# Performance work log

Hardware: AMD Instinct MI355X
Metric: run time of the kernel (lower is better)

## Reference

```python
import jax, jax.numpy as jnp
import numpy as np

N, D, V, T = 1024, 64, 32000, 2048
U_DECAY = 0.97
LN_EPS = 1e-6


def _layernorm_row(z):
    # matches torch: (z - mean) / (std_unbiased + eps), std uses ddof=1
    m = z.mean(axis=-1, keepdims=True)
    s = jnp.std(z, axis=-1, ddof=1, keepdims=True)
    return (z - m) / (s + LN_EPS)


def setup_inputs() -> dict:
    key = jax.random.key(0)
    k1, k2, k3, k4, k5 = jax.random.split(key, 5)
    E = jax.random.normal(k1, (D, N), dtype=jnp.float32) / np.float32(np.sqrt(N))
    Dx = jax.random.normal(k2, (N, D), dtype=jnp.float32) / np.float32(np.sqrt(D))
    Dy = jax.random.normal(k3, (N, D), dtype=jnp.float32) / np.float32(np.sqrt(D))
    token_emb = jax.random.normal(k4, (V, D), dtype=jnp.float32) / np.float32(np.sqrt(D))
    tokens = jax.random.randint(k5, (T,), 0, V, dtype=jnp.int32)
    x0 = jnp.zeros((N,), dtype=jnp.float32)
    rho0 = jnp.zeros((D, N), dtype=jnp.float32)
    return {"E": E, "Dx": Dx, "Dy": Dy, "token_emb": token_emb,
            "x0": x0, "rho0": rho0, "tokens": tokens}


def reference(E, Dx, Dy, token_emb, x0, rho0, tokens):
    def step(carry, tok):
        x, rho = carry                        # x: [N], rho: [D, N]
        v_prev = token_emb[tok]               # [D]
        x_t = x + jax.nn.relu(Dx @ v_prev)    # [N], use_relu_lowrank=True
        a_star = rho @ x_t                    # [D]
        y_core = Dy @ _layernorm_row(a_star)  # ln_before_Dy=True -> [N]
        y_t = jax.nn.relu(y_core) * jax.nn.relu(x_t)  # [N]
        v_star = _layernorm_row(E @ y_t)      # [D]
        rho_new = U_DECAY * (rho + jnp.outer(v_prev, x_t))  # [D, N]
        return (x_t, rho_new), (y_t, v_star)

    (_, _), (ys, vs) = jax.lax.scan(step, (x0, rho0), tokens)
    return ys, vs  # [T, N], [T, D]
```

## Files before the change

kernel.cpp:

```cpp
#include <hip/hip_runtime.h>
#include <math.h>

#define NN 1024
#define DD 64
#define TT 2048
#define UDEC 0.97f
#define EPS 1e-6f

#define CC 64
#define NCH 32
#define NSL 16
#define SLW 64
#define C2 8
#define NC2 256

#define NTHR 256

__device__ __forceinline__ int swz4(int r, int c4) { return r * 16 + (c4 ^ (r & 15)); }

#define DOT4(p, q2) ((p).x*(q2).x + (p).y*(q2).y + (p).z*(q2).z + (p).w*(q2).w)
#define F4ADD(a, b) make_float4((a).x+(b).x, (a).y+(b).y, (a).z+(b).z, (a).w+(b).w)

__global__ __launch_bounds__(NTHR) void k_xscan(
    const float* __restrict__ Dx, const float* __restrict__ temb,
    const int* __restrict__ toks, float* __restrict__ Xp, float* __restrict__ S)
{
    __shared__ float Vs[C2][DD];
    const int b = blockIdx.x, tid = threadIdx.x;
    const int cs = b >> 2, qx = b & 3;
    const int n = qx * 256 + tid;
    for (int i = tid; i < C2 * DD / 4; i += NTHR) {
        int s = i >> 4, d4 = i & 15;
        reinterpret_cast<float4*>(&Vs[s][0])[d4] =
            reinterpret_cast<const float4*>(temb + toks[cs * C2 + s] * DD)[d4];
    }
    __syncthreads();
    float dxr[DD];
    const float4* dx4 = reinterpret_cast<const float4*>(Dx + n * DD);
#pragma unroll
    for (int j = 0; j < 16; ++j) {
        float4 v = dx4[j];
        dxr[4*j] = v.x; dxr[4*j+1] = v.y; dxr[4*j+2] = v.z; dxr[4*j+3] = v.w;
    }
    float run = 0.f;
    for (int s = 0; s < C2; ++s) {
        const float4* vr = reinterpret_cast<const float4*>(&Vs[s][0]);
        float a0 = 0.f, a1 = 0.f, a2 = 0.f, a3 = 0.f;
#pragma unroll
        for (int j = 0; j < 16; ++j) {
            float4 v = vr[j];
            a0 += v.x * dxr[4*j];     a1 += v.y * dxr[4*j+1];
            a2 += v.z * dxr[4*j+2];   a3 += v.w * dxr[4*j+3];
        }
        run += fmaxf((a0 + a1) + (a2 + a3), 0.f);
        Xp[(cs * C2 + s) * NN + n] = run;
    }
    S[cs * NN + n] = run;
}

__global__ __launch_bounds__(NTHR) void k_base(
    const float* __restrict__ S, const float* __restrict__ x0, float* __restrict__ Bb,
    const float* __restrict__ E, float* __restrict__ Et4)
{
    const int b = blockIdx.x, tid = threadIdx.x;
    if (b < 32) {
        __shared__ float ssl[8][33];
        const int n_l = tid & 31, seg = tid >> 5;
        const int n = b * 32 + n_l;
        float m[32];
#pragma unroll
        for (int j = 0; j < 32; ++j) m[j] = S[(seg * 32 + j) * NN + n];
        float tot = 0.f;
#pragma unroll
        for (int j = 0; j < 32; ++j) tot += m[j];
        ssl[seg][n_l] = tot;
        __syncthreads();
        float acc = x0[n];
        for (int r = 0; r < seg; ++r) acc += ssl[r][n_l];
#pragma unroll
        for (int j = 0; j < 32; ++j) {
            Bb[(seg * 32 + j) * NN + n] = acc;
            acc += m[j];
        }
    } else {
        const int fi = (b - 32) * NTHR + tid;
        const int n4 = fi >> 6, d = fi & 63;
        reinterpret_cast<float4*>(Et4)[fi] =
            reinterpret_cast<const float4*>(E)[d * (NN / 4) + n4];
    }
}

__global__ __launch_bounds__(NTHR) void k_mgram(
    const float* __restrict__ Xp, const float* __restrict__ Bb,
    const float* __restrict__ temb, const int* __restrict__ toks,
    float* __restrict__ M, float* __restrict__ Gp)
{
    __shared__ float Xs[CC * DD];
    __shared__ float Vw[CC * DD];
    __shared__ float pw[CC + 1];
    const int b = blockIdx.x, tid = threadIdx.x;
    const int c = b >> 5, q = (b >> 1) & 15, role = b & 1;
    if (role == 0 && tid <= CC) pw[tid] = powf(UDEC, (float)tid);
    for (int i = tid; i < CC * SLW / 4; i += NTHR) {
        int s = i >> 4, n4 = i & 15;
        int t = c * CC + s;
        float4 xv = *reinterpret_cast<const float4*>(&Xp[t * NN + q * SLW + n4 * 4]);
        float4 bv = *reinterpret_cast<const float4*>(&Bb[(t >> 3) * NN + q * SLW + n4 * 4]);
        reinterpret_cast<float4*>(Xs)[swz4(s, n4)] = F4ADD(xv, bv);
    }
    __syncthreads();
    if (role == 0) {
        for (int i = tid; i < CC * DD / 4; i += NTHR) {
            int s = i >> 4, d4 = i & 15;
            float4 v = reinterpret_cast<const float4*>(temb + toks[c * CC + s] * DD)[d4];
            float wv = pw[CC - s];
            reinterpret_cast<float4*>(Vw)[swz4(s, d4)] =
                make_float4(v.x * wv, v.y * wv, v.z * wv, v.w * wv);
        }
    }
    __syncthreads();
    const float4* Xs4 = reinterpret_cast<const float4*>(Xs);
    if (role == 0) {
        const int dg = tid >> 4, ng = tid & 15;
        float acc[16];
#pragma unroll
        for (int k = 0; k < 16; ++k) acc[k] = 0.f;
        const float4* Vw4 = reinterpret_cast<const float4*>(Vw);
        for (int s = 0; s < CC; ++s) {
            float4 vw = Vw4[swz4(s, dg)];
            float4 xs = Xs4[swz4(s, ng)];
            acc[0]  += vw.x*xs.x; acc[1]  += vw.x*xs.y; acc[2]  += vw.x*xs.z; acc[3]  += vw.x*xs.w;
            acc[4]  += vw.y*xs.x; acc[5]  += vw.y*xs.y; acc[6]  += vw.y*xs.z; acc[7]  += vw.y*xs.w;
            acc[8]  += vw.z*xs.x; acc[9]  += vw.z*xs.y; acc[10] += vw.z*xs.z; acc[11] += vw.z*xs.w;
            acc[12] += vw.w*xs.x; acc[13] += vw.w*xs.y; acc[14] += vw.w*xs.z; acc[15] += vw.w*xs.w;
        }
#pragma unroll
        for (int a = 0; a < 4; ++a)
            *reinterpret_cast<float4*>(&M[(c * DD + dg * 4 + a) * NN + q * SLW + ng * 4]) =
                make_float4(acc[a*4], acc[a*4+1], acc[a*4+2], acc[a*4+3]);
    } else {
        const int tg = tid >> 4, sg = tid & 15;
        float acc[16];
#pragma unroll
        for (int k = 0; k < 16; ++k) acc[k] = 0.f;
        for (int n4 = 0; n4 < 16; ++n4) {
            float4 xa[4], xb[4];
#pragma unroll
            for (int a = 0; a < 4; ++a) xa[a] = Xs4[swz4(tg * 4 + a, n4)];
#pragma unroll
            for (int e = 0; e < 4; ++e) xb[e] = Xs4[swz4(sg * 4 + e, n4)];
#pragma unroll
            for (int a = 0; a < 4; ++a)
#pragma unroll
                for (int e = 0; e < 4; ++e) acc[a*4+e] += DOT4(xa[a], xb[e]);
        }
        float* base = Gp + ((size_t)(c * NSL + q) * CC) * CC;
#pragma unroll
        for (int a = 0; a < 4; ++a)
            *reinterpret_cast<float4*>(base + (tg * 4 + a) * CC + sg * 4) =
                make_float4(acc[a*4], acc[a*4+1], acc[a*4+2], acc[a*4+3]);
    }
}

__global__ __launch_bounds__(NTHR) void k_rho(
    const float* __restrict__ M, const float* __restrict__ rho0, float* __restrict__ Rho)
{
    __shared__ float4 ssl[8][32];
    const int b = blockIdx.x, tid = threadIdx.x;
    const int l = tid & 31, seg = tid >> 5;
    const int f = b * 32 + l;
    const float uc  = powf(UDEC, (float)CC);
    const float uc4 = uc * uc * uc * uc;
    const float4* M4 = reinterpret_cast<const float4*>(M);
    float4 mreg[4];
#pragma unroll
    for (int j = 0; j < 4; ++j) mreg[j] = M4[(size_t)(seg * 4 + j) * (DD * NN / 4) + f];
    float4 ss = mreg[0];
#pragma unroll
    for (int j = 1; j < 4; ++j) {
        ss.x = fmaf(ss.x, uc, mreg[j].x); ss.y = fmaf(ss.y, uc, mreg[j].y);
        ss.z = fmaf(ss.z, uc, mreg[j].z); ss.w = fmaf(ss.w, uc, mreg[j].w);
    }
    ssl[seg][l] = ss;
    __syncthreads();
    float4 acc = reinterpret_cast<const float4*>(rho0)[f];
    for (int r = 0; r < seg; ++r) {
        float4 sv = ssl[r][l];
        acc.x = fmaf(acc.x, uc4, sv.x); acc.y = fmaf(acc.y, uc4, sv.y);
        acc.z = fmaf(acc.z, uc4, sv.z); acc.w = fmaf(acc.w, uc4, sv.w);
    }
    float4* R4 = reinterpret_cast<float4*>(Rho);
#pragma unroll
    for (int j = 0; j < 4; ++j) {
        R4[(size_t)(seg * 4 + j) * (DD * NN / 4) + f] = acc;
        acc.x = fmaf(acc.x, uc, mreg[j].x); acc.y = fmaf(acc.y, uc, mreg[j].y);
        acc.z = fmaf(acc.z, uc, mreg[j].z); acc.w = fmaf(acc.w, uc, mreg[j].w);
    }
}

__global__ __launch_bounds__(NTHR) void k_inter(
    const float* __restrict__ Xp, const float* __restrict__ Bb,
    const float* __restrict__ Rho, float* __restrict__ Pp)
{
    __shared__ float Xs[32 * DD];
    __shared__ float Rs[DD * DD];
    const int b = blockIdx.x, tid = threadIdx.x;
    const int c = b >> 5, q = (b >> 1) & 15, h = b & 1;
    for (int i = tid; i < 32 * SLW / 4; i += NTHR) {
        int s = i >> 4, n4 = i & 15;
        int t = c * CC + h * 32 + s;
        float4 xv = *reinterpret_cast<const float4*>(&Xp[t * NN + q * SLW + n4 * 4]);
        float4 bv = *reinterpret_cast<const float4*>(&Bb[(t >> 3) * NN + q * SLW + n4 * 4]);
        reinterpret_cast<float4*>(Xs)[swz4(s, n4)] = F4ADD(xv, bv);
    }
    for (int i = tid; i < DD * SLW / 4; i += NTHR) {
        int s = i >> 4, n4 = i & 15;
        reinterpret_cast<float4*>(Rs)[swz4(s, n4)] =
            *reinterpret_cast<const float4*>(&Rho[(size_t)(c * DD + s) * NN + q * SLW + n4 * 4]);
    }
    __syncthreads();
    const float4* Xs4 = reinterpret_cast<const float4*>(Xs);
    const float4* Rs4 = reinterpret_cast<const float4*>(Rs);
    const int ti = tid >> 4, dg = tid & 15;
    float acc[8];
#pragma unroll
    for (int k = 0; k < 8; ++k) acc[k] = 0.f;
    for (int n4 = 0; n4 < 16; ++n4) {
        float4 xa[2], rv[4];
#pragma unroll
        for (int a = 0; a < 2; ++a) xa[a] = Xs4[swz4(ti * 2 + a, n4)];
#pragma unroll
        for (int e = 0; e < 4; ++e) rv[e] = Rs4[swz4(dg * 4 + e, n4)];
#pragma unroll
        for (int a = 0; a < 2; ++a)
#pragma unroll
            for (int e = 0; e < 4; ++e) acc[a*4+e] += DOT4(xa[a], rv[e]);
    }
#pragma unroll
    for (int a = 0; a < 2; ++a) {
        int trow = h * 32 + ti * 2 + a;
        *reinterpret_cast<float4*>(
            Pp + (((size_t)(c * NSL + q) * CC) + trow) * DD + dg * 4) =
            make_float4(acc[a*4], acc[a*4+1], acc[a*4+2], acc[a*4+3]);
    }
}

__global__ __launch_bounds__(NTHR) void k_astar(
    const float* __restrict__ Gp, const float* __restrict__ Pp,
    const float* __restrict__ temb, const int* __restrict__ toks,
    float* __restrict__ LNA)
{
    __shared__ float Ve[CC * DD];
    __shared__ float Gt[4][CC];
    __shared__ float Pt[4][DD];
    __shared__ float pw[CC + 1];
    const int b = blockIdx.x, tid = threadIdx.x;
    const int c = b >> 4, sub = b & 15;
    if (tid <= CC) pw[tid] = powf(UDEC, (float)tid);
    for (int i = tid; i < CC * DD / 4; i += NTHR) {
        int s = i >> 4, d4 = i & 15;
        reinterpret_cast<float4*>(Ve)[s * 16 + d4] =
            reinterpret_cast<const float4*>(temb + toks[c * CC + s] * DD)[d4];
    }
    {
        int k = tid >> 6, s = tid & 63;
        int t = sub + 16 * k;
        float ag = 0.f, ap = 0.f;
#pragma unroll
        for (int q = 0; q < NSL; ++q) {
            ag += Gp[((size_t)(c * NSL + q) * CC + t) * CC + s];
            ap += Pp[((size_t)(c * NSL + q) * CC + t) * DD + s];
        }
        Gt[k][s] = ag; Pt[k][s] = ap;
    }
    __syncthreads();
    {
        const int tk = tid >> 6, d0 = tid & 63;
        const int t = sub + 16 * tk;
        float a = pw[t] * Pt[tk][d0];
        for (int s = 0; s < t; ++s)
            a = fmaf(pw[t - s] * Gt[tk][s], Ve[s * 64 + d0], a);
        float sum = a;
#pragma unroll
        for (int mm = 1; mm < 64; mm <<= 1) sum += __shfl_xor(sum, mm, 64);
        float mean = sum * (1.f / DD);
        float z = a - mean;
        float vv = z * z;
#pragma unroll
        for (int mm = 1; mm < 64; mm <<= 1) vv += __shfl_xor(vv, mm, 64);
        float inv = 1.f / (sqrtf(vv * (1.f / (DD - 1))) + EPS);
        LNA[(c * CC + t) * DD + d0] = z * inv;
    }
}

__global__ __launch_bounds__(NTHR) void k_y(
    const float* __restrict__ LNA, const float* __restrict__ Dy,
    const float* __restrict__ Xp, const float* __restrict__ Bb,
    float* __restrict__ ys)
{
    __shared__ float L[8][DD];
    const int tt = blockIdx.y;
    const int n  = blockIdx.x * 256 + threadIdx.x;
    for (int i = threadIdx.x; i < 8 * DD / 4; i += NTHR)
        reinterpret_cast<float4*>(&L[0][0])[i] =
            reinterpret_cast<const float4*>(LNA + tt * 8 * DD)[i];
    __syncthreads();
    float dyr[DD];
    const float4* dy4 = reinterpret_cast<const float4*>(Dy + n * DD);
#pragma unroll
    for (int j = 0; j < 16; ++j) {
        float4 v = dy4[j];
        dyr[4*j] = v.x; dyr[4*j+1] = v.y; dyr[4*j+2] = v.z; dyr[4*j+3] = v.w;
    }
#pragma unroll
    for (int t = 0; t < 8; ++t) {
        const float4* lr = reinterpret_cast<const float4*>(&L[t][0]);
        float a0 = 0.f, a1 = 0.f, a2 = 0.f, a3 = 0.f;
#pragma unroll
        for (int j = 0; j < 16; ++j) {
            float4 v = lr[j];
            a0 += v.x * dyr[4*j];   a1 += v.y * dyr[4*j+1];
            a2 += v.z * dyr[4*j+2]; a3 += v.w * dyr[4*j+3];
        }
        float yc = (a0 + a1) + (a2 + a3);
        int tg = tt * 8 + t;
        float xv = Xp[tg * NN + n] + Bb[(tg >> 3) * NN + n];
        ys[tg * NN + n] = fmaxf(yc, 0.f) * fmaxf(xv, 0.f);
    }
}

__global__ __launch_bounds__(NTHR) void k_v(
    const float* __restrict__ ys, const float* __restrict__ Et4, float* __restrict__ vs)
{
    __shared__ float Ys[4][NN];
    __shared__ float pre4[4][4][DD];
    __shared__ float pre[4][DD + 1];
    __shared__ float mrow[4], srow[4];
    const int tt = blockIdx.x, tid = threadIdx.x;
    for (int i = tid; i < NN; i += NTHR)
        reinterpret_cast<float4*>(&Ys[0][0])[i] =
            reinterpret_cast<const float4*>(ys + (size_t)tt * 4 * NN)[i];
    __syncthreads();
    const int w = tid >> 6, d = tid & 63;
    float a0 = 0.f, a1 = 0.f, a2 = 0.f, a3 = 0.f;
    const float4* et = reinterpret_cast<const float4*>(Et4) + (size_t)w * 64 * DD + d;
#pragma unroll 4
    for (int i = 0; i < 64; ++i) {
        float4 ev = et[(size_t)i * DD];
        const int n4g = (w * 64 + i) * 4;
        float4 y0 = *reinterpret_cast<const float4*>(&Ys[0][n4g]);
        float4 y1 = *reinterpret_cast<const float4*>(&Ys[1][n4g]);
        float4 y2 = *reinterpret_cast<const float4*>(&Ys[2][n4g]);
        float4 y3 = *reinterpret_cast<const float4*>(&Ys[3][n4g]);
        a0 += DOT4(ev, y0); a1 += DOT4(ev, y1);
        a2 += DOT4(ev, y2); a3 += DOT4(ev, y3);
    }
    pre4[w][0][d] = a0; pre4[w][1][d] = a1;
    pre4[w][2][d] = a2; pre4[w][3][d] = a3;
    __syncthreads();
    {
        const int k = tid >> 6, dd = tid & 63;
        pre[k][dd] = pre4[0][k][dd] + pre4[1][k][dd] + pre4[2][k][dd] + pre4[3][k][dd];
    }
    __syncthreads();
    if (tid < 4) {
        float m = 0.f;
#pragma unroll
        for (int dd2 = 0; dd2 < DD; ++dd2) m += pre[tid][dd2];
        m *= (1.f / DD);
        float v = 0.f;
#pragma unroll
        for (int dd2 = 0; dd2 < DD; ++dd2) { float z = pre[tid][dd2] - m; v += z * z; }
        mrow[tid] = m;
        srow[tid] = 1.f / (sqrtf(v * (1.f / (DD - 1))) + EPS);
    }
    __syncthreads();
    {
        int k = tid >> 6, dd = tid & 63;
        vs[(tt * 4 + k) * DD + dd] = (pre[k][dd] - mrow[k]) * srow[k];
    }
}

extern "C" void kernel_launch(void* const* d_in, const int* in_sizes, int n_in,
                              void* d_out, int out_size, void* d_ws, size_t ws_size,
                              hipStream_t stream) {
    (void)in_sizes; (void)n_in; (void)out_size; (void)ws_size;
    const float* E    = (const float*)d_in[0];
    const float* Dx   = (const float*)d_in[1];
    const float* Dy   = (const float*)d_in[2];
    const float* temb = (const float*)d_in[3];
    const float* x0   = (const float*)d_in[4];
    const float* rho0 = (const float*)d_in[5];
    const int*   toks = (const int*)d_in[6];

    float* ys = (float*)d_out;
    float* vs = ys + (size_t)TT * NN;

    float* w   = (float*)d_ws;
    float* Xp  = w;
    float* S   = Xp  + (size_t)TT * NN;
    float* Bb  = S   + (size_t)NC2 * NN;
    float* M   = Bb  + (size_t)NC2 * NN;
    float* Rho = M   + (size_t)NCH * DD * NN;
    float* Gp  = Rho + (size_t)NCH * DD * NN;
    float* LNA = Gp  + (size_t)NCH * NSL * CC * CC;
    float* Et4 = LNA + (size_t)TT * DD;
    float* Pp  = M;

    k_xscan<<<dim3(4 * NC2),   NTHR, 0, stream>>>(Dx, temb, toks, Xp, S);
    k_base <<<dim3(96),        NTHR, 0, stream>>>(S, x0, Bb, E, Et4);
    k_mgram<<<dim3(NCH*NSL*2), NTHR, 0, stream>>>(Xp, Bb, temb, toks, M, Gp);
    k_rho  <<<dim3(512),       NTHR, 0, stream>>>(M, rho0, Rho);
    k_inter<<<dim3(NCH*NSL*2), NTHR, 0, stream>>>(Xp, Bb, Rho, Pp);
    k_astar<<<dim3(NCH*16),    NTHR, 0, stream>>>(Gp, Pp, temb, toks, LNA);
    k_y    <<<dim3(4, TT/8),   NTHR, 0, stream>>>(LNA, Dy, Xp, Bb, ys);
    k_v    <<<dim3(TT/4),      NTHR, 0, stream>>>(ys, Et4, vs);
}
```

Baseline: 167.8 us.

## Fuse y and v kernels and pre-transpose Dx/Dy for coalesced loads

Adds a prep kernel that transposes Dx and Dy into a d4-major layout, so the per-thread row loads in the x-scan and y stages become coalesced across threads. The E transpose moves into that prep kernel, which leaves k_base as a pure prefix-sum kernel. The y and v stages are fused into one kernel: each block computes four time steps of ys for all N, keeps them in shared memory and immediately reduces them with E, which avoids re-reading ys from global memory and saves one launch. In exchange, each fused block reloads all of Dy (four passes over n), and there is an extra launch plus workspace for the transposed copies.

```diff
diff --git a/kernel.cpp b/kernel.cpp
--- a/kernel.cpp
+++ b/kernel.cpp
@@ -21,8 +21,32 @@
 #define DOT4(p, q2) ((p).x*(q2).x + (p).y*(q2).y + (p).z*(q2).z + (p).w*(q2).w)
 #define F4ADD(a, b) make_float4((a).x+(b).x, (a).y+(b).y, (a).z+(b).z, (a).w+(b).w)
 
+__global__ __launch_bounds__(NTHR) void k_prep(
+    const float* __restrict__ E, float* __restrict__ Et4,
+    const float* __restrict__ Dx, float* __restrict__ Dxq,
+    const float* __restrict__ Dy, float* __restrict__ Dyq)
+{
+    const int b = blockIdx.x, tid = threadIdx.x;
+    if (b < 64) {
+        const int fi = b * NTHR + tid;
+        const int n4 = fi >> 6, d = fi & 63;
+        reinterpret_cast<float4*>(Et4)[fi] =
+            reinterpret_cast<const float4*>(E)[d * (NN / 4) + n4];
+    } else if (b < 128) {
+        const int fi = (b - 64) * NTHR + tid;
+        const int d4 = fi >> 10, n = fi & 1023;
+        reinterpret_cast<float4*>(Dxq)[fi] =
+            reinterpret_cast<const float4*>(Dx)[n * (DD / 4) + d4];
+    } else {
+        const int fi = (b - 128) * NTHR + tid;
+        const int d4 = fi >> 10, n = fi & 1023;
+        reinterpret_cast<float4*>(Dyq)[fi] =
+            reinterpret_cast<const float4*>(Dy)[n * (DD / 4) + d4];
+    }
+}
+
 __global__ __launch_bounds__(NTHR) void k_xscan(
-    const float* __restrict__ Dx, const float* __restrict__ temb,
+    const float* __restrict__ Dxq, const float* __restrict__ temb,
     const int* __restrict__ toks, float* __restrict__ Xp, float* __restrict__ S)
 {
     __shared__ float Vs[C2][DD];
@@ -36,10 +60,10 @@
     }
     __syncthreads();
     float dxr[DD];
-    const float4* dx4 = reinterpret_cast<const float4*>(Dx + n * DD);
+    const float4* dxq4 = reinterpret_cast<const float4*>(Dxq);
 #pragma unroll
     for (int j = 0; j < 16; ++j) {
-        float4 v = dx4[j];
+        float4 v = dxq4[j * NN + n];
         dxr[4*j] = v.x; dxr[4*j+1] = v.y; dxr[4*j+2] = v.z; dxr[4*j+3] = v.w;
     }
     float run = 0.f;
@@ -59,34 +83,26 @@
 }
 
 __global__ __launch_bounds__(NTHR) void k_base(
-    const float* __restrict__ S, const float* __restrict__ x0, float* __restrict__ Bb,
-    const float* __restrict__ E, float* __restrict__ Et4)
-{
-    const int b = blockIdx.x, tid = threadIdx.x;
-    if (b < 32) {
-        __shared__ float ssl[8][33];
-        const int n_l = tid & 31, seg = tid >> 5;
-        const int n = b * 32 + n_l;
-        float m[32];
-#pragma unroll
-        for (int j = 0; j < 32; ++j) m[j] = S[(seg * 32 + j) * NN + n];
-        float tot = 0.f;
-#pragma unroll
-        for (int j = 0; j < 32; ++j) tot += m[j];
-        ssl[seg][n_l] = tot;
-        __syncthreads();
-        float acc = x0[n];
-        for (int r = 0; r < seg; ++r) acc += ssl[r][n_l];
-#pragma unroll
-        for (int j = 0; j < 32; ++j) {
-            Bb[(seg * 32 + j) * NN + n] = acc;
-            acc += m[j];
-        }
-    } else {
-        const int fi = (b - 32) * NTHR + tid;
-        const int n4 = fi >> 6, d = fi & 63;
-        reinterpret_cast<float4*>(Et4)[fi] =
-            reinterpret_cast<const float4*>(E)[d * (NN / 4) + n4];
+    const float* __restrict__ S, const float* __restrict__ x0, float* __restrict__ Bb)
+{
+    __shared__ float ssl[8][33];
+    const int b = blockIdx.x, tid = threadIdx.x;
+    const int n_l = tid & 31, seg = tid >> 5;
+    const int n = b * 32 + n_l;
+    float m[32];
+#pragma unroll
+    for (int j = 0; j < 32; ++j) m[j] = S[(seg * 32 + j) * NN + n];
+    float tot = 0.f;
+#pragma unroll
+    for (int j = 0; j < 32; ++j) tot += m[j];
+    ssl[seg][n_l] = tot;
+    __syncthreads();
+    float acc = x0[n];
+    for (int r = 0; r < seg; ++r) acc += ssl[r][n_l];
+#pragma unroll
+    for (int j = 0; j < 32; ++j) {
+        Bb[(seg * 32 + j) * NN + n] = acc;
+        acc += m[j];
     }
 }
 
@@ -293,53 +309,49 @@
     }
 }
 
-__global__ __launch_bounds__(NTHR) void k_y(
-    const float* __restrict__ LNA, const float* __restrict__ Dy,
+__global__ __launch_bounds__(NTHR) void k_yv(
+    const float* __restrict__ LNA, const float* __restrict__ Dyq,
     const float* __restrict__ Xp, const float* __restrict__ Bb,
-    float* __restrict__ ys)
-{
-    __shared__ float L[8][DD];
-    const int tt = blockIdx.y;
-    const int n  = blockIdx.x * 256 + threadIdx.x;
-    for (int i = threadIdx.x; i < 8 * DD / 4; i += NTHR)
-        reinterpret_cast<float4*>(&L[0][0])[i] =
-            reinterpret_cast<const float4*>(LNA + tt * 8 * DD)[i];
-    __syncthreads();
-    float dyr[DD];
-    const float4* dy4 = reinterpret_cast<const float4*>(Dy + n * DD);
-#pragma unroll
-    for (int j = 0; j < 16; ++j) {
-        float4 v = dy4[j];
-        dyr[4*j] = v.x; dyr[4*j+1] = v.y; dyr[4*j+2] = v.z; dyr[4*j+3] = v.w;
-    }
-#pragma unroll
-    for (int t = 0; t < 8; ++t) {
-        const float4* lr = reinterpret_cast<const float4*>(&L[t][0]);
-        float a0 = 0.f, a1 = 0.f, a2 = 0.f, a3 = 0.f;
-#pragma unroll
-        for (int j = 0; j < 16; ++j) {
-            float4 v = lr[j];
-            a0 += v.x * dyr[4*j];   a1 += v.y * dyr[4*j+1];
-            a2 += v.z * dyr[4*j+2]; a3 += v.w * dyr[4*j+3];
-        }
-        float yc = (a0 + a1) + (a2 + a3);
-        int tg = tt * 8 + t;
-        float xv = Xp[tg * NN + n] + Bb[(tg >> 3) * NN + n];
-        ys[tg * NN + n] = fmaxf(yc, 0.f) * fmaxf(xv, 0.f);
-    }
-}
-
-__global__ __launch_bounds__(NTHR) void k_v(
-    const float* __restrict__ ys, const float* __restrict__ Et4, float* __restrict__ vs)
-{
+    const float* __restrict__ Et4, float* __restrict__ ys, float* __restrict__ vs)
+{
+    __shared__ float L[4][DD];
     __shared__ float Ys[4][NN];
     __shared__ float pre4[4][4][DD];
     __shared__ float pre[4][DD + 1];
     __shared__ float mrow[4], srow[4];
     const int tt = blockIdx.x, tid = threadIdx.x;
-    for (int i = tid; i < NN; i += NTHR)
-        reinterpret_cast<float4*>(&Ys[0][0])[i] =
-            reinterpret_cast<const float4*>(ys + (size_t)tt * 4 * NN)[i];
+    if (tid < 64) {
+        reinterpret_cast<float4*>(&L[0][0])[tid] =
+            reinterpret_cast<const float4*>(LNA + tt * 4 * DD)[tid];
+    }
+    __syncthreads();
+    const float4* dyq4 = reinterpret_cast<const float4*>(Dyq);
+    for (int nq = 0; nq < 4; ++nq) {
+        const int n = nq * 256 + tid;
+        float dyr[DD];
+#pragma unroll
+        for (int j = 0; j < 16; ++j) {
+            float4 v = dyq4[j * NN + n];
+            dyr[4*j] = v.x; dyr[4*j+1] = v.y; dyr[4*j+2] = v.z; dyr[4*j+3] = v.w;
+        }
+#pragma unroll
+        for (int k = 0; k < 4; ++k) {
+            const float4* lr = reinterpret_cast<const float4*>(&L[k][0]);
+            float a0 = 0.f, a1 = 0.f, a2 = 0.f, a3 = 0.f;
+#pragma unroll
+            for (int j = 0; j < 16; ++j) {
+                float4 v = lr[j];
+                a0 += v.x * dyr[4*j];   a1 += v.y * dyr[4*j+1];
+                a2 += v.z * dyr[4*j+2]; a3 += v.w * dyr[4*j+3];
+            }
+            float yc = (a0 + a1) + (a2 + a3);
+            int tg = tt * 4 + k;
+            float xv = Xp[tg * NN + n] + Bb[(tg >> 3) * NN + n];
+            float yv = fmaxf(yc, 0.f) * fmaxf(xv, 0.f);
+            ys[tg * NN + n] = yv;
+            Ys[k][n] = yv;
+        }
+    }
     __syncthreads();
     const int w = tid >> 6, d = tid & 63;
     float a0 = 0.f, a1 = 0.f, a2 = 0.f, a3 = 0.f;
@@ -405,14 +417,16 @@
     float* Gp  = Rho + (size_t)NCH * DD * NN;
     float* LNA = Gp  + (size_t)NCH * NSL * CC * CC;
     float* Et4 = LNA + (size_t)TT * DD;
+    float* Dxq = Et4 + (size_t)NN * DD;
+    float* Dyq = Dxq + (size_t)NN * DD;
     float* Pp  = M;
 
-    k_xscan<<<dim3(4 * NC2),   NTHR, 0, stream>>>(Dx, temb, toks, Xp, S);
-    k_base <<<dim3(96),        NTHR, 0, stream>>>(S, x0, Bb, E, Et4);
+    k_prep <<<dim3(192),       NTHR, 0, stream>>>(E, Et4, Dx, Dxq, Dy, Dyq);
+    k_xscan<<<dim3(4 * NC2),   NTHR, 0, stream>>>(Dxq, temb, toks, Xp, S);
+    k_base <<<dim3(32),        NTHR, 0, stream>>>(S, x0, Bb);
     k_mgram<<<dim3(NCH*NSL*2), NTHR, 0, stream>>>(Xp, Bb, temb, toks, M, Gp);
     k_rho  <<<dim3(512),       NTHR, 0, stream>>>(M, rho0, Rho);
     k_inter<<<dim3(NCH*NSL*2), NTHR, 0, stream>>>(Xp, Bb, Rho, Pp);
     k_astar<<<dim3(NCH*16),    NTHR, 0, stream>>>(Gp, Pp, temb, toks, LNA);
-    k_y    <<<dim3(4, TT/8),   NTHR, 0, stream>>>(LNA, Dy, Xp, Bb, ys);
-    k_v    <<<dim3(TT/4),      NTHR, 0, stream>>>(ys, Et4, vs);
-}
+    k_yv   <<<dim3(TT/4),      NTHR, 0, stream>>>(LNA, Dyq, Xp, Bb, Et4, ys, vs);
+}
```

New measurement: 180.9 us. 7.8% more time.
